# Kernel optimization log

Hardware: AMD Instinct MI355X
Metric: run time of the kernel (lower is better)

## Reference

```python
import jax, jax.numpy as jnp
import numpy as np

NEG_SLOPE = 0.2


def setup_inputs() -> dict:
    key = jax.random.key(0)
    ks = jax.random.split(key, 9)
    N, E, D, H, C, G = 50000, 800000, 128, 4, 32, 64
    x = jax.random.normal(ks[0], (N, D), dtype=jnp.float32)
    edge_index = jax.random.randint(ks[1], (2, E), 0, N, dtype=jnp.int64)
    batch_ids = jnp.sort(jax.random.randint(ks[2], (N,), 0, G, dtype=jnp.int64))
    Wl = jax.random.normal(ks[3], (D, H * C), dtype=jnp.float32) / np.sqrt(D)
    Wr = jax.random.normal(ks[4], (D, H * C), dtype=jnp.float32) / np.sqrt(D)
    att = jax.random.normal(ks[5], (H, C), dtype=jnp.float32) / np.sqrt(C)
    bias_conv = jax.random.normal(ks[6], (H * C,), dtype=jnp.float32) * 0.01
    W_mlp = jax.random.normal(ks[7], (H * C, H * C), dtype=jnp.float32) / np.sqrt(H * C)
    b_mlp = jax.random.normal(ks[8], (H * C,), dtype=jnp.float32) * 0.01
    return {"x": x, "edge_index": edge_index, "batch_ids": batch_ids,
            "num_graphs": G, "Wl": Wl, "Wr": Wr, "att": att,
            "bias_conv": bias_conv, "W_mlp": W_mlp, "b_mlp": b_mlp}


def gatv2_forward(x, edge_index, batch_ids, num_graphs, Wl, Wr, att, bias_conv, W_mlp, b_mlp):
    N = x.shape[0]
    H, C = att.shape
    # add self loops (PyG default)
    loops = jnp.arange(N, dtype=edge_index.dtype)
    src = jnp.concatenate([edge_index[0], loops])
    dst = jnp.concatenate([edge_index[1], loops])
    xl = (x @ Wl).reshape(N, H, C)  # source transform
    xr = (x @ Wr).reshape(N, H, C)  # target transform
    # GATv2 attention logits per edge/head
    e = jax.nn.leaky_relu(xl[src] + xr[dst], NEG_SLOPE)  # [E,H,C]
    logits = jnp.einsum('ehc,hc->eh', e, att)            # [E,H]
    # segment softmax over incoming edges of each dst node
    m = jax.ops.segment_max(logits, dst, num_segments=N)
    ex = jnp.exp(logits - m[dst])
    denom = jax.ops.segment_sum(ex, dst, num_segments=N)
    alpha = ex / denom[dst]                              # [E,H]
    # weighted scatter-sum of source features
    out = jax.ops.segment_sum(alpha[:, :, None] * xl[src], dst, num_segments=N)
    out = out.reshape(N, H * C) + bias_conv
    out = jax.nn.relu(out)
    # global max pool per graph
    pooled = jax.ops.segment_max(out, batch_ids, num_segments=num_graphs)
    return jax.nn.relu(pooled @ W_mlp + b_mlp)


def reference(x, edge_index, batch_ids, num_graphs, Wl, Wr, att, bias_conv, W_mlp, b_mlp):
    return gatv2_forward(x, edge_index, batch_ids, num_graphs, Wl, Wr, att,
                         bias_conv, W_mlp, b_mlp)
```

## Files before the change

kernel.cpp:

```cpp
#include <hip/hip_runtime.h>
#include <hip/hip_bf16.h>

#define NN 50000
#define EE 800000
#define HC 128
#define GG 64

#define NBLK 256
#define CHUNK (EE / NBLK)
#define NBUCK ((NN + 63) >> 6)
#define NTOT (NBUCK * NBLK)
#define NSB ((NTOT + 1023) / 1024)
#define ECAP 2048

typedef __attribute__((ext_vector_type(8))) short bf16x8;
typedef __attribute__((ext_vector_type(4))) float f32x4;
typedef _Float16 hv2 __attribute__((ext_vector_type(2)));

__device__ __forceinline__ float dpp4_redrow(float t) {
  t += __int_as_float(__builtin_amdgcn_update_dpp(0, __float_as_int(t), 0x111, 0xf, 0xf, true));
  t += __int_as_float(__builtin_amdgcn_update_dpp(0, __float_as_int(t), 0x112, 0xf, 0xf, true));
  t += __int_as_float(__builtin_amdgcn_update_dpp(0, __float_as_int(t), 0x114, 0xf, 0xf, true));
  t += __int_as_float(__builtin_amdgcn_update_dpp(0, __float_as_int(t), 0x118, 0xf, 0xf, true));
  return t;
}
__device__ __forceinline__ float bcast15(float t) {
  return __int_as_float(__builtin_amdgcn_ds_swizzle(__float_as_int(t), 0x1F0));
}

__device__ __forceinline__ unsigned pkbf(float lo, float hi) {
  __hip_bfloat162 h = __float22bfloat162_rn(float2{lo, hi});
  return *reinterpret_cast<unsigned*>(&h);
}

__global__ __launch_bounds__(128) void prep_w(const float* __restrict__ Wl,
                                              const float* __restrict__ Wr,
                                              short* __restrict__ Wtb) {
  int c = blockIdx.x;
  int k = threadIdx.x;
  const float* W = (c < 128) ? Wl : Wr;
  float v = W[k * 128 + (c & 127)];
  Wtb[c * 128 + k] = (short)(pkbf(v, 0.f) & 0xFFFF);
}

__global__ __launch_bounds__(256) void gemm_xw(
    const float* __restrict__ x, const short* __restrict__ Wtb,
    _Float16* __restrict__ xlh, _Float16* __restrict__ xrh)
{
  __shared__ short xs[128 * 136];
  const int t = threadIdx.x;
  const int rowbase = blockIdx.x * 128;
#pragma unroll
  for (int i = 0; i < 16; ++i) {
    int fi = i * 256 + t;
    int row = fi >> 5, k4 = fi & 31;
    int ar = rowbase + row; if (ar >= NN) ar = NN - 1;
    float4 v = *(const float4*)(x + (size_t)ar * 128 + k4 * 4);
    uint2 p = { pkbf(v.x, v.y), pkbf(v.z, v.w) };
    *(uint2*)&xs[row * 136 + k4 * 4] = p;
  }
  __syncthreads();
  const int w = t >> 6, l = t & 63;
  const int lo16 = l & 15, hi = l >> 4;
  f32x4 accL[2][8], accR[2][8];
#pragma unroll
  for (int rf = 0; rf < 2; ++rf)
#pragma unroll
    for (int cf = 0; cf < 8; ++cf) {
      accL[rf][cf] = f32x4{0.f, 0.f, 0.f, 0.f};
      accR[rf][cf] = f32x4{0.f, 0.f, 0.f, 0.f};
    }

  const short* asrc0 = &xs[(w * 32 + lo16) * 136 + hi * 8];
  const short* asrc1 = asrc0 + 16 * 136;
#pragma unroll
  for (int ks = 0; ks < 4; ++ks) {
    bf16x8 a0 = *(const bf16x8*)(asrc0 + ks * 32);
    bf16x8 a1 = *(const bf16x8*)(asrc1 + ks * 32);
#pragma unroll
    for (int cf = 0; cf < 8; ++cf) {
      const short* bp = &Wtb[(cf * 16 + lo16) * 128 + ks * 32 + hi * 8];
      bf16x8 bL = *(const bf16x8*)bp;
      bf16x8 bR = *(const bf16x8*)(bp + 128 * 128);
      accL[0][cf] = __builtin_amdgcn_mfma_f32_16x16x32_bf16(a0, bL, accL[0][cf], 0, 0, 0);
      accL[1][cf] = __builtin_amdgcn_mfma_f32_16x16x32_bf16(a1, bL, accL[1][cf], 0, 0, 0);
      accR[0][cf] = __builtin_amdgcn_mfma_f32_16x16x32_bf16(a0, bR, accR[0][cf], 0, 0, 0);
      accR[1][cf] = __builtin_amdgcn_mfma_f32_16x16x32_bf16(a1, bR, accR[1][cf], 0, 0, 0);
    }
  }
#pragma unroll
  for (int rf = 0; rf < 2; ++rf)
#pragma unroll
    for (int cf = 0; cf < 8; ++cf)
#pragma unroll
      for (int r = 0; r < 4; ++r) {
        int row = rowbase + w * 32 + rf * 16 + hi * 4 + r;
        if (row < NN) {
          int col = cf * 16 + lo16;
          xlh[(size_t)row * 128 + col] = (_Float16)accL[rf][cf][r];
          xrh[(size_t)row * 128 + col] = (_Float16)accR[rf][cf][r];
        }
      }
}

__global__ __launch_bounds__(256) void hist_coarse(const int* __restrict__ ei,
                                                   int* __restrict__ H2T) {
  __shared__ int h[NBUCK];
  int t = threadIdx.x, blk = blockIdx.x;
  for (int b = t; b < NBUCK; b += 256) h[b] = 0;
  __syncthreads();
  int e0 = blk * CHUNK;
  for (int i = t; i < CHUNK; i += 256) {
    int d = ei[EE + e0 + i];
    atomicAdd(&h[d >> 6], 1);
  }
  __syncthreads();
  for (int b = t; b < NBUCK; b += 256) H2T[b * NBLK + blk] = h[b];
}

__global__ __launch_bounds__(256) void scanA(const int* __restrict__ H2T,
                                             int* __restrict__ PS, int* __restrict__ bsum) {
  __shared__ int tmp[256];
  int t = threadIdx.x;
  int base = blockIdx.x * 1024 + t * 4;
  int4 v = {0, 0, 0, 0};
  if (base < NTOT) v = *(const int4*)&H2T[base];
  int local = v.x + v.y + v.z + v.w;
  tmp[t] = local; __syncthreads();
  for (int off = 1; off < 256; off <<= 1) {
    int xv = (t >= off) ? tmp[t - off] : 0; __syncthreads();
    tmp[t] += xv; __syncthreads();
  }
  int excl = tmp[t] - local;
  if (base < NTOT) {
    int4 o;
    o.x = excl; excl += v.x;
    o.y = excl; excl += v.y;
    o.z = excl; excl += v.z;
    o.w = excl;
    *(int4*)&PS[base] = o;
  }
  if (t == 255) bsum[blockIdx.x] = tmp[255];
}

__global__ void scanB(int* __restrict__ bsum) {
  __shared__ int tmp[256];
  int t = threadIdx.x;
  int v = (t < NSB) ? bsum[t] : 0;
  tmp[t] = v; __syncthreads();
  for (int off = 1; off < 256; off <<= 1) {
    int xv = (t >= off) ? tmp[t - off] : 0; __syncthreads();
    tmp[t] += xv; __syncthreads();
  }
  if (t < NSB) bsum[t] = tmp[t] - v;
}

__global__ __launch_bounds__(256) void scatter_coarse(const int* __restrict__ ei,
                                                      const int* __restrict__ PS,
                                                      const int* __restrict__ bsum,
                                                      int* __restrict__ ec) {
  __shared__ int colbase[NBUCK];
  __shared__ int cur[NBUCK];
  int t = threadIdx.x, blk = blockIdx.x;
  for (int b = t; b < NBUCK; b += 256) {
    int L = b * NBLK + blk;
    colbase[b] = PS[L] + bsum[L >> 10];
    cur[b] = 0;
  }
  __syncthreads();
  int e0 = blk * CHUNK;
  for (int i = t; i < CHUNK; i += 256) {
    int d = ei[EE + e0 + i], s = ei[e0 + i];
    int b = d >> 6;
    int r = atomicAdd(&cur[b], 1);
    ec[colbase[b] + r] = s | ((d & 63) << 16);
  }
}

__global__ __launch_bounds__(256) void fine_sort(const int* __restrict__ PS,
                                                 const int* __restrict__ bsum,
                                                 const int* __restrict__ ec,
                                                 int* __restrict__ rs, int* __restrict__ csr) {
  __shared__ int lbuf[ECAP];
  __shared__ int outb[ECAP + 64];
  __shared__ int fh[64], sexcl[65], cur2[64];
  int t = threadIdx.x, b = blockIdx.x;
  int L0 = b * NBLK;
  int start = PS[L0] + bsum[L0 >> 10];
  int end = (b + 1 < NBUCK) ? PS[L0 + NBLK] + bsum[(L0 + NBLK) >> 10] : EE;
  int node0 = b << 6;
  int nl = NN - node0; if (nl > 64) nl = 64;
  int cnt = end - start; if (cnt > ECAP) cnt = ECAP;
  if (t < 64) { fh[t] = 0; cur2[t] = 0; }
  __syncthreads();
  for (int i = t; i < cnt; i += 256) {
    int p = ec[start + i];
    lbuf[i] = p;
    atomicAdd(&fh[(p >> 16) & 63], 1);
  }
  __syncthreads();
  if (t < 64) {
    int val = fh[t] + (t < nl ? 1 : 0);
    int w = val;
    for (int off = 1; off < 64; off <<= 1) {
      int u = __shfl_up(w, off);
      if (t >= off) w += u;
    }
    sexcl[t] = w - val;
    if (t == 63) sexcl[64] = w;
  }
  __syncthreads();
  int base = start + node0;
  if (t <= nl) rs[node0 + t] = base + sexcl[t];
  if (t < nl) {
    int r = atomicAdd(&cur2[t], 1);
    outb[sexcl[t] + r] = node0 + t;
  }
  for (int i = t; i < cnt; i += 256) {
    int p = lbuf[i];
    int f = (p >> 16) & 63;
    int r = atomicAdd(&cur2[f], 1);
    outb[sexcl[f] + r] = p & 0xFFFF;
  }
  __syncthreads();
  int tot = cnt + nl;
  for (int i = t; i < tot; i += 256) csr[base + i] = outb[i];
}

__device__ __forceinline__ void proc8(const unsigned* wv, hv2 att2, hv2 xr2,
                                      float& s, float& a0, float& a1) {
  float tb[8];
#pragma unroll
  for (int i = 0; i < 8; ++i) {
    hv2 v = __builtin_bit_cast(hv2, wv[i]);
    hv2 y = v + xr2;
    hv2 lr = __builtin_elementwise_max(y, y * (_Float16)0.2f);
    float td = __builtin_amdgcn_fdot2(lr, att2, 0.f, false);
    tb[i] = bcast15(dpp4_redrow(td));
  }
  float p[8];
#pragma unroll
  for (int i = 0; i < 8; ++i) p[i] = __builtin_amdgcn_exp2f(tb[i]);
#pragma unroll
  for (int i = 0; i < 8; ++i) {
    hv2 v = __builtin_bit_cast(hv2, wv[i]);
    s += p[i];
    a0 = fmaf(p[i], (float)v.x, a0);
    a1 = fmaf(p[i], (float)v.y, a1);
  }
}

__global__ __launch_bounds__(256) void gat_agg(
    const unsigned* __restrict__ xlu, const unsigned* __restrict__ xru,
    const int* __restrict__ rs, const int* __restrict__ csr,
    const float* __restrict__ att, const float* __restrict__ bias,
    float* __restrict__ outn)
{
  int wid = threadIdx.x >> 6, lane = threadIdx.x & 63;
  int n = blockIdx.x * 4 + wid;
  if (n >= NN) return;
  hv2 xr2 = __builtin_bit_cast(hv2, xru[n * 64 + lane]);
  float2 at2 = ((const float2*)att)[lane];
  const float LOG2E = 1.4426950408889634f;
  hv2 att2;
  att2.x = (_Float16)(at2.x * LOG2E);
  att2.y = (_Float16)(at2.y * LOG2E);
  float s = 0.f, a0 = 0.f, a1 = 0.f;

  int jbeg = rs[n], jend = rs[n + 1];
  for (int j0 = jbeg; j0 < jend; j0 += 64) {
    int cnt = jend - j0; if (cnt > 64) cnt = 64;
    int sj = csr[j0 + (lane < cnt ? lane : cnt - 1)];
    int base = 0;
    if (cnt >= 8) {
      unsigned cur[8];
#pragma unroll
      for (int i = 0; i < 8; ++i)
        cur[i] = xlu[__builtin_amdgcn_readlane(sj, i) * 64 + lane];
      for (; base + 16 <= cnt; base += 8) {
        unsigned nxt[8];
#pragma unroll
        for (int i = 0; i < 8; ++i)
          nxt[i] = xlu[__builtin_amdgcn_readlane(sj, base + 8 + i) * 64 + lane];
        proc8(cur, att2, xr2, s, a0, a1);
#pragma unroll
        for (int i = 0; i < 8; ++i) cur[i] = nxt[i];
      }
      proc8(cur, att2, xr2, s, a0, a1);
      base += 8;
    }
    for (; base < cnt; ++base) {
      unsigned w0 = xlu[__builtin_amdgcn_readlane(sj, base) * 64 + lane];
      hv2 va = __builtin_bit_cast(hv2, w0);
      hv2 ya = va + xr2;
      hv2 la = __builtin_elementwise_max(ya, ya * (_Float16)0.2f);
      float t = __builtin_amdgcn_fdot2(la, att2, 0.f, false);
      float p = __builtin_amdgcn_exp2f(bcast15(dpp4_redrow(t)));
      s += p;
      a0 = fmaf(p, (float)va.x, a0); a1 = fmaf(p, (float)va.y, a1);
    }
  }
  float inv = 1.f / s;
  float2 bi = ((const float2*)bias)[lane];
  float2 o;
  o.x = fmaxf(fmaf(a0, inv, bi.x), 0.f);
  o.y = fmaxf(fmaf(a1, inv, bi.y), 0.f);
  ((float2*)outn)[n * 64 + lane] = o;
}

__global__ __launch_bounds__(1024) void pool_mlp(const float* __restrict__ outn,
                                                 const int* __restrict__ batch,
                                                 const float* __restrict__ W,
                                                 const float* __restrict__ bm,
                                                 float* __restrict__ out) {
  __shared__ float pm[8][128];
  __shared__ float p[128];
  __shared__ float acc8[8][128];
  int g = blockIdx.x, t = threadIdx.x;
  int c = t & 127, q = t >> 7;
  int a = 0, bnd = NN;
  while (a < bnd) { int m = (a + bnd) >> 1; if (batch[m] < g) a = m + 1; else bnd = m; }
  int lo = a;
  bnd = NN;
  while (a < bnd) { int m = (a + bnd) >> 1; if (batch[m] < g + 1) a = m + 1; else bnd = m; }
  int hi = a;
  float mx = 0.f;
#pragma unroll 4
  for (int n = lo + q; n < hi; n += 8) mx = fmaxf(mx, outn[(size_t)n * 128 + c]);
  pm[q][c] = mx;
  __syncthreads();
  if (q == 0) {
    float m0 = pm[0][c];
#pragma unroll
    for (int i = 1; i < 8; ++i) m0 = fmaxf(m0, pm[i][c]);
    p[c] = m0;
  }
  __syncthreads();
  float acc = 0.f;
#pragma unroll
  for (int kk = 0; kk < 16; ++kk) {
    int k = q * 16 + kk;
    acc = fmaf(p[k], W[k * 128 + c], acc);
  }
  acc8[q][c] = acc;
  __syncthreads();
  if (q == 0) {
    float sum = bm[c];
#pragma unroll
    for (int i = 0; i < 8; ++i) sum += acc8[i][c];
    out[g * 128 + c] = fmaxf(sum, 0.f);
  }
}

extern "C" void kernel_launch(void* const* d_in, const int* in_sizes, int n_in,
                              void* d_out, int out_size, void* d_ws, size_t ws_size,
                              hipStream_t stream) {
  const float* x    = (const float*)d_in[0];
  const int*   ei   = (const int*)d_in[1];
  const int*   batch= (const int*)d_in[2];
  const float* Wl   = (const float*)d_in[4];
  const float* Wr   = (const float*)d_in[5];
  const float* att  = (const float*)d_in[6];
  const float* bias = (const float*)d_in[7];
  const float* Wm   = (const float*)d_in[8];
  const float* bm   = (const float*)d_in[9];

  char* ws = (char*)d_ws;
  size_t off = 0;
  auto alloc = [&](size_t bytes) { void* p = ws + off; off += (bytes + 255) & ~size_t(255); return p; };
  unsigned* xlu  = (unsigned*)alloc((size_t)NN * 64 * 4);
  unsigned* xru  = (unsigned*)alloc((size_t)NN * 64 * 4);
  float* outn    = (float*)alloc((size_t)NN * HC * 4);
  int*   rs      = (int*)alloc((size_t)(NN + 1) * 4);
  int*   csr     = (int*)alloc((size_t)(EE + NN) * 4);
  int*   H2T     = (int*)alloc((size_t)NTOT * 4);
  int*   PS      = (int*)alloc((size_t)NTOT * 4);
  int*   ec      = (int*)alloc((size_t)EE * 4);
  int*   bsum    = (int*)alloc(NSB * 4);
  short* Wtb     = (short*)alloc((size_t)256 * 128 * 2);

  prep_w<<<256, 128, 0, stream>>>(Wl, Wr, Wtb);
  gemm_xw<<<(NN + 127) / 128, 256, 0, stream>>>(x, Wtb, (_Float16*)xlu, (_Float16*)xru);
  hist_coarse<<<NBLK, 256, 0, stream>>>(ei, H2T);
  scanA<<<NSB, 256, 0, stream>>>(H2T, PS, bsum);
  scanB<<<1, 256, 0, stream>>>(bsum);
  scatter_coarse<<<NBLK, 256, 0, stream>>>(ei, PS, bsum, ec);
  fine_sort<<<NBUCK, 256, 0, stream>>>(PS, bsum, ec, rs, csr);
  gat_agg<<<NN / 4, 256, 0, stream>>>(xlu, xru, rs, csr, att, bias, outn);
  pool_mlp<<<GG, 1024, 0, stream>>>(outn, batch, Wm, bm, (float*)d_out);
}
```

Measured before the change: 137.2 us.

## Fuse histogram into GEMM, inline block-sum scan, batch tail edge processing

The coarse destination histogram moves into the first 256 blocks of the GEMM kernel, and the single-block scanB launch goes away: each scatter_coarse and fine_sort block now redoes the small block-sum prefix scan in shared memory. Together these remove two kernel launches and the serial gaps between them. The leftover edges after the 8-wide loop in the aggregation kernel are now loaded together and handled by one templated batch, replacing a serial per-edge loop, so their loads and exps can overlap. In exchange, every scatter and sort block pays a redundant scan, and the GEMM blocks carry extra shared memory and edge reads.

```diff
diff --git a/kernel.cpp b/kernel.cpp
--- a/kernel.cpp
+++ b/kernel.cpp
@@ -45,9 +45,11 @@
 
 __global__ __launch_bounds__(256) void gemm_xw(
     const float* __restrict__ x, const short* __restrict__ Wtb,
-    _Float16* __restrict__ xlh, _Float16* __restrict__ xrh)
+    _Float16* __restrict__ xlh, _Float16* __restrict__ xrh,
+    const int* __restrict__ ei, int* __restrict__ H2T)
 {
   __shared__ short xs[128 * 136];
+  __shared__ int h[NBUCK];
   const int t = threadIdx.x;
   const int rowbase = blockIdx.x * 128;
 #pragma unroll
@@ -101,21 +103,18 @@
           xrh[(size_t)row * 128 + col] = (_Float16)accR[rf][cf][r];
         }
       }
-}
-
-__global__ __launch_bounds__(256) void hist_coarse(const int* __restrict__ ei,
-                                                   int* __restrict__ H2T) {
-  __shared__ int h[NBUCK];
-  int t = threadIdx.x, blk = blockIdx.x;
-  for (int b = t; b < NBUCK; b += 256) h[b] = 0;
-  __syncthreads();
-  int e0 = blk * CHUNK;
-  for (int i = t; i < CHUNK; i += 256) {
-    int d = ei[EE + e0 + i];
-    atomicAdd(&h[d >> 6], 1);
-  }
-  __syncthreads();
-  for (int b = t; b < NBUCK; b += 256) H2T[b * NBLK + blk] = h[b];
+  int blk = blockIdx.x;
+  if (blk < NBLK) {
+    for (int b = t; b < NBUCK; b += 256) h[b] = 0;
+    __syncthreads();
+    int e0 = blk * CHUNK;
+    for (int i = t; i < CHUNK; i += 256) {
+      int d = ei[EE + e0 + i];
+      atomicAdd(&h[d >> 6], 1);
+    }
+    __syncthreads();
+    for (int b = t; b < NBUCK; b += 256) H2T[b * NBLK + blk] = h[b];
+  }
 }
 
 __global__ __launch_bounds__(256) void scanA(const int* __restrict__ H2T,
@@ -143,28 +142,26 @@
   if (t == 255) bsum[blockIdx.x] = tmp[255];
 }
 
-__global__ void scanB(int* __restrict__ bsum) {
-  __shared__ int tmp[256];
-  int t = threadIdx.x;
-  int v = (t < NSB) ? bsum[t] : 0;
-  tmp[t] = v; __syncthreads();
-  for (int off = 1; off < 256; off <<= 1) {
-    int xv = (t >= off) ? tmp[t - off] : 0; __syncthreads();
-    tmp[t] += xv; __syncthreads();
-  }
-  if (t < NSB) bsum[t] = tmp[t] - v;
-}
-
 __global__ __launch_bounds__(256) void scatter_coarse(const int* __restrict__ ei,
                                                       const int* __restrict__ PS,
                                                       const int* __restrict__ bsum,
                                                       int* __restrict__ ec) {
   __shared__ int colbase[NBUCK];
   __shared__ int cur[NBUCK];
+  __shared__ int sb[NSB];
+  __shared__ int stmp[256];
   int t = threadIdx.x, blk = blockIdx.x;
+  int v = (t < NSB) ? bsum[t] : 0;
+  stmp[t] = v; __syncthreads();
+  for (int off = 1; off < 256; off <<= 1) {
+    int xv = (t >= off) ? stmp[t - off] : 0; __syncthreads();
+    stmp[t] += xv; __syncthreads();
+  }
+  if (t < NSB) sb[t] = stmp[t] - v;
+  __syncthreads();
   for (int b = t; b < NBUCK; b += 256) {
     int L = b * NBLK + blk;
-    colbase[b] = PS[L] + bsum[L >> 10];
+    colbase[b] = PS[L] + sb[L >> 10];
     cur[b] = 0;
   }
   __syncthreads();
@@ -184,10 +181,20 @@
   __shared__ int lbuf[ECAP];
   __shared__ int outb[ECAP + 64];
   __shared__ int fh[64], sexcl[65], cur2[64];
+  __shared__ int sb[NSB];
+  __shared__ int stmp[256];
   int t = threadIdx.x, b = blockIdx.x;
+  int v = (t < NSB) ? bsum[t] : 0;
+  stmp[t] = v; __syncthreads();
+  for (int off = 1; off < 256; off <<= 1) {
+    int xv = (t >= off) ? stmp[t - off] : 0; __syncthreads();
+    stmp[t] += xv; __syncthreads();
+  }
+  if (t < NSB) sb[t] = stmp[t] - v;
+  __syncthreads();
   int L0 = b * NBLK;
-  int start = PS[L0] + bsum[L0 >> 10];
-  int end = (b + 1 < NBUCK) ? PS[L0 + NBLK] + bsum[(L0 + NBLK) >> 10] : EE;
+  int start = PS[L0] + sb[L0 >> 10];
+  int end = (b + 1 < NBUCK) ? PS[L0 + NBLK] + sb[(L0 + NBLK) >> 10] : EE;
   int node0 = b << 6;
   int nl = NN - node0; if (nl > 64) nl = 64;
   int cnt = end - start; if (cnt > ECAP) cnt = ECAP;
@@ -227,22 +234,23 @@
   for (int i = t; i < tot; i += 256) csr[base + i] = outb[i];
 }
 
-__device__ __forceinline__ void proc8(const unsigned* wv, hv2 att2, hv2 xr2,
+template<int M>
+__device__ __forceinline__ void procM(const unsigned* wv, hv2 att2, hv2 xr2,
                                       float& s, float& a0, float& a1) {
-  float tb[8];
-#pragma unroll
-  for (int i = 0; i < 8; ++i) {
+  float tb[M];
+#pragma unroll
+  for (int i = 0; i < M; ++i) {
     hv2 v = __builtin_bit_cast(hv2, wv[i]);
     hv2 y = v + xr2;
     hv2 lr = __builtin_elementwise_max(y, y * (_Float16)0.2f);
     float td = __builtin_amdgcn_fdot2(lr, att2, 0.f, false);
     tb[i] = bcast15(dpp4_redrow(td));
   }
-  float p[8];
-#pragma unroll
-  for (int i = 0; i < 8; ++i) p[i] = __builtin_amdgcn_exp2f(tb[i]);
-#pragma unroll
-  for (int i = 0; i < 8; ++i) {
+  float p[M];
+#pragma unroll
+  for (int i = 0; i < M; ++i) p[i] = __builtin_amdgcn_exp2f(tb[i]);
+#pragma unroll
+  for (int i = 0; i < M; ++i) {
     hv2 v = __builtin_bit_cast(hv2, wv[i]);
     s += p[i];
     a0 = fmaf(p[i], (float)v.x, a0);
@@ -282,22 +290,28 @@
 #pragma unroll
         for (int i = 0; i < 8; ++i)
           nxt[i] = xlu[__builtin_amdgcn_readlane(sj, base + 8 + i) * 64 + lane];
-        proc8(cur, att2, xr2, s, a0, a1);
+        procM<8>(cur, att2, xr2, s, a0, a1);
 #pragma unroll
         for (int i = 0; i < 8; ++i) cur[i] = nxt[i];
       }
-      proc8(cur, att2, xr2, s, a0, a1);
+      procM<8>(cur, att2, xr2, s, a0, a1);
       base += 8;
     }
-    for (; base < cnt; ++base) {
-      unsigned w0 = xlu[__builtin_amdgcn_readlane(sj, base) * 64 + lane];
-      hv2 va = __builtin_bit_cast(hv2, w0);
-      hv2 ya = va + xr2;
-      hv2 la = __builtin_elementwise_max(ya, ya * (_Float16)0.2f);
-      float t = __builtin_amdgcn_fdot2(la, att2, 0.f, false);
-      float p = __builtin_amdgcn_exp2f(bcast15(dpp4_redrow(t)));
-      s += p;
-      a0 = fmaf(p, (float)va.x, a0); a1 = fmaf(p, (float)va.y, a1);
+    int rem = cnt - base;
+    if (rem) {
+      unsigned wv[8];
+#pragma unroll
+      for (int i = 0; i < 8; ++i)
+        if (i < rem) wv[i] = xlu[__builtin_amdgcn_readlane(sj, base + i) * 64 + lane];
+      switch (rem) {
+        case 1: procM<1>(wv, att2, xr2, s, a0, a1); break;
+        case 2: procM<2>(wv, att2, xr2, s, a0, a1); break;
+        case 3: procM<3>(wv, att2, xr2, s, a0, a1); break;
+        case 4: procM<4>(wv, att2, xr2, s, a0, a1); break;
+        case 5: procM<5>(wv, att2, xr2, s, a0, a1); break;
+        case 6: procM<6>(wv, att2, xr2, s, a0, a1); break;
+        default: procM<7>(wv, att2, xr2, s, a0, a1); break;
+      }
     }
   }
   float inv = 1.f / s;
@@ -380,10 +394,8 @@
   short* Wtb     = (short*)alloc((size_t)256 * 128 * 2);
 
   prep_w<<<256, 128, 0, stream>>>(Wl, Wr, Wtb);
-  gemm_xw<<<(NN + 127) / 128, 256, 0, stream>>>(x, Wtb, (_Float16*)xlu, (_Float16*)xru);
-  hist_coarse<<<NBLK, 256, 0, stream>>>(ei, H2T);
+  gemm_xw<<<(NN + 127) / 128, 256, 0, stream>>>(x, Wtb, (_Float16*)xlu, (_Float16*)xru, ei, H2T);
   scanA<<<NSB, 256, 0, stream>>>(H2T, PS, bsum);
-  scanB<<<1, 256, 0, stream>>>(bsum);
   scatter_coarse<<<NBLK, 256, 0, stream>>>(ei, PS, bsum, ec);
   fine_sort<<<NBUCK, 256, 0, stream>>>(PS, bsum, ec, rs, csr);
   gat_agg<<<NN / 4, 256, 0, stream>>>(xlu, xru, rs, csr, att, bias, outn);
```

Measured after the change: 135.1 us. Within noise of the previous version (-1.5%).
